# Kernel tuning notes

Measured on AMD Instinct MI355X. Metric: run time of the kernel, lower is better.

Reference implementation:

```python
import jax, jax.numpy as jnp
import numpy as np

B, N, E, H = 8, 2000, 20, 128


def setup_inputs() -> dict:
    key = jax.random.key(0)
    ks = jax.random.split(key, 9)
    s = 1.0 / np.sqrt(H)
    return {
        "x": jax.random.normal(ks[0], (B, N, H), dtype=jnp.float32),
        "e": jax.random.normal(ks[1], (B, N * E, H), dtype=jnp.float32),
        "Wu": jax.random.uniform(ks[2], (H, H), jnp.float32, -s, s),
        "bu": jax.random.uniform(ks[3], (H,), jnp.float32, -s, s),
        "Wv": jax.random.uniform(ks[4], (H, H), jnp.float32, -s, s),
        "bv": jax.random.uniform(ks[5], (H,), jnp.float32, -s, s),
        "We": jax.random.uniform(ks[6], (H, H), jnp.float32, -s, s),
        "be": jax.random.uniform(ks[7], (H,), jnp.float32, -s, s),
        "edge_index": jax.random.randint(ks[8], (B, N * E), 0, N, dtype=jnp.int32),
        "n_edges": E,
    }


def reference(x, e, Wu, bu, Wv, bv, We, be, edge_index, n_edges):
    b, n, h = x.shape
    Ux = x @ Wu + bu                      # [B, N, H] node self-embedding
    Vx = x @ Wv + bv                      # [B, N, H] neighbor embedding
    Ve = e @ We + be                      # [B, N*E, H] edge embedding
    # softmax over the n_edges axis per (node, channel)
    Ve = jax.nn.softmax(Ve.reshape(b, n, n_edges, h), axis=2)
    # gather neighbor features along node axis via edge_index
    Vx_g = jnp.take_along_axis(Vx, edge_index[..., None], axis=1)  # [B, N*E, H]
    to = (Ve * Vx_g.reshape(b, n, n_edges, h)).sum(axis=2)          # [B, N, H]
    return Ux + to
```

## Files before the change

kernel.cpp:

```cpp
#include <hip/hip_runtime.h>

#define B_   8
#define NN   2000
#define EE   20
#define HH   128
#define BN   (B_*NN)
#define NE   (NN*EE)

typedef unsigned short ushort_t;
typedef __bf16 bf16x8 __attribute__((ext_vector_type(8)));
typedef float  f32x4  __attribute__((ext_vector_type(4)));
typedef float  f4     __attribute__((ext_vector_type(4)));
typedef unsigned short us8 __attribute__((ext_vector_type(8)));
typedef unsigned short us4 __attribute__((ext_vector_type(4)));

union FragU { us8 u; bf16x8 b; };

__device__ __forceinline__ float b2f(ushort_t v) {
    union { unsigned int i; float f; } c; c.i = ((unsigned int)v) << 16; return c.f;
}
__device__ __forceinline__ ushort_t f2b(float f) {
    union { float f; unsigned int i; } c; c.f = f;
    unsigned int r = (c.i + 0x7FFFu + ((c.i >> 16) & 1u)) >> 16;
    return (ushort_t)r;
}

__global__ __launch_bounds__(256) void k0_prep(
    const float* __restrict__ x,
    const float* __restrict__ Wu, const float* __restrict__ Wv,
    const float* __restrict__ We,
    ushort_t* __restrict__ xb,
    ushort_t* __restrict__ WuT, ushort_t* __restrict__ WvT,
    ushort_t* __restrict__ WeT)
{
    const int bid = blockIdx.x;
    if (bid < 125) {
        const size_t base = (size_t)bid * 128 * HH;
#pragma unroll
        for (int it = 0; it < 16; ++it) {
            int c = it * 256 + threadIdx.x;
            size_t off = base + (size_t)c * 4;
            f4 v = *(const f4*)(x + off);
            us4 pk;
#pragma unroll
            for (int r = 0; r < 4; ++r) pk[r] = f2b(v[r]);
            *(us4*)(xb + off) = pk;
        }
    } else {
        const float* W = (bid == 125) ? Wu : (bid == 126) ? Wv : We;
        ushort_t*   WT = (bid == 125) ? WuT : (bid == 126) ? WvT : WeT;
#pragma unroll
        for (int it = 0; it < 64; ++it) {
            int c = it * 256 + threadIdx.x;
            int k = c >> 7, n = c & 127;
            WT[n * HH + k] = f2b(W[c]);
        }
    }
}

__global__ __launch_bounds__(256, 4) void k1_embed(
    const ushort_t* __restrict__ xb,
    const ushort_t* __restrict__ WuT, const float* __restrict__ bu,
    const ushort_t* __restrict__ WvT, const float* __restrict__ bv,
    ushort_t* __restrict__ Uxb, ushort_t* __restrict__ Vxb)
{
    const int tid  = threadIdx.x;
    const int lane = tid & 63;
    const int wave = tid >> 6;
    const int wm = wave >> 1, wn = wave & 1;
    const int q  = lane >> 4, ln = lane & 15;
    const int m0 = blockIdx.x * 64;
    const int sel = blockIdx.y;
    const ushort_t* WT   = sel ? WvT : WuT;
    const float*    bias = sel ? bv : bu;
    ushort_t* dst = sel ? Vxb : Uxb;

    f32x4 acc[2][4];
#pragma unroll
    for (int tm = 0; tm < 2; ++tm)
#pragma unroll
        for (int tn = 0; tn < 4; ++tn) acc[tm][tn] = (f32x4){0.f, 0.f, 0.f, 0.f};

#pragma unroll
    for (int ki = 0; ki < 4; ++ki) {
        FragU af[2], bf[4];
#pragma unroll
        for (int tm = 0; tm < 2; ++tm)
            af[tm].u = *(const us8*)(xb + (size_t)(m0 + wm * 32 + tm * 16 + ln) * HH + ki * 32 + q * 8);
#pragma unroll
        for (int tn = 0; tn < 4; ++tn)
            bf[tn].u = *(const us8*)(WT + (size_t)(wn * 64 + tn * 16 + ln) * HH + ki * 32 + q * 8);
#pragma unroll
        for (int tm = 0; tm < 2; ++tm)
#pragma unroll
            for (int tn = 0; tn < 4; ++tn)
                acc[tm][tn] = __builtin_amdgcn_mfma_f32_16x16x32_bf16(
                    af[tm].b, bf[tn].b, acc[tm][tn], 0, 0, 0);
    }

#pragma unroll
    for (int tn = 0; tn < 4; ++tn) {
        int col = wn * 64 + tn * 16 + ln;
        float bb = bias[col];
#pragma unroll
        for (int tm = 0; tm < 2; ++tm) {
            int rowb = m0 + wm * 32 + tm * 16 + q * 4;
#pragma unroll
            for (int r = 0; r < 4; ++r)
                dst[(size_t)(rowb + r) * HH + col] = f2b(acc[tm][tn][r] + bb);
        }
    }
}

#define ASTR 136
#define CSTR 84

__global__ __launch_bounds__(256, 4) void k2_fused(
    const float* __restrict__ e, const ushort_t* __restrict__ WeT,
    const int* __restrict__ eidx,
    const ushort_t* __restrict__ Uxb, const ushort_t* __restrict__ Vxb,
    float* __restrict__ out)
{
    __shared__ __align__(16) ushort_t smem[11008];
    __shared__ int sidx[80];

    const int tid  = threadIdx.x;
    const int lane = tid & 63;
    const int wave = tid >> 6;
    const int q  = lane >> 4, ln = lane & 15;

    const int b   = blockIdx.y;
    const int nl0 = blockIdx.x * 4;
    const size_t erow0 = (size_t)b * NE + (size_t)nl0 * EE;

#pragma unroll
    for (int it = 0; it < 10; ++it) {
        int c = it * 256 + tid;
        int row = c >> 5, col = (c & 31) * 4;
        f4 v = *(const f4*)(e + (erow0 + row) * HH + col);
        us4 pk;
#pragma unroll
        for (int r = 0; r < 4; ++r) pk[r] = f2b(v[r]);
        *(us4*)(&smem[row * ASTR + col]) = pk;
    }
    if (tid < 80) sidx[tid] = eidx[erow0 + tid];

    FragU bf[4][2];
#pragma unroll
    for (int ki = 0; ki < 4; ++ki)
#pragma unroll
        for (int tn = 0; tn < 2; ++tn)
            bf[ki][tn].u = *(const us8*)(WeT + (size_t)(wave * 32 + tn * 16 + ln) * HH + ki * 32 + q * 8);

    f32x4 acc[5][2];
#pragma unroll
    for (int tm = 0; tm < 5; ++tm)
#pragma unroll
        for (int tn = 0; tn < 2; ++tn) acc[tm][tn] = (f32x4){0.f, 0.f, 0.f, 0.f};

    __syncthreads();

#pragma unroll
    for (int ki = 0; ki < 4; ++ki) {
        FragU af[5];
#pragma unroll
        for (int tm = 0; tm < 5; ++tm)
            af[tm].u = *(const us8*)(&smem[(tm * 16 + ln) * ASTR + ki * 32 + q * 8]);
#pragma unroll
        for (int tm = 0; tm < 5; ++tm)
#pragma unroll
            for (int tn = 0; tn < 2; ++tn)
                acc[tm][tn] = __builtin_amdgcn_mfma_f32_16x16x32_bf16(
                    af[tm].b, bf[ki][tn].b, acc[tm][tn], 0, 0, 0);
    }

    __syncthreads();

#pragma unroll
    for (int tm = 0; tm < 5; ++tm)
#pragma unroll
        for (int tn = 0; tn < 2; ++tn) {
            int col  = wave * 32 + tn * 16 + ln;
            int rowb = tm * 16 + q * 4;
            us4 pk;
#pragma unroll
            for (int r = 0; r < 4; ++r) pk[r] = f2b(acc[tm][tn][r]);
            *(us4*)(&smem[col * CSTR + rowb]) = pk;
        }


    const int hh = lane & 31;
    const int gh = lane >> 5;
    const int h  = wave * 32 + hh;
    const ushort_t* vbase = Vxb + (size_t)b * NN * HH + h;
#pragma unroll
    for (int j = 0; j < 2; ++j) {
        int g = gh + 2 * j;
        const ushort_t* ctp = &smem[h * CSTR + g * 20];
        float lv[20];
#pragma unroll
        for (int i = 0; i < 5; ++i) {
            us4 v = *(const us4*)(ctp + i * 4);
#pragma unroll
            for (int r = 0; r < 4; ++r) lv[i * 4 + r] = b2f(v[r]);
        }
        float mx = lv[0];
#pragma unroll
        for (int k = 1; k < EE; ++k) mx = fmaxf(mx, lv[k]);

        ushort_t gv[20];
        const int ib = g * 20;
#pragma unroll
        for (int k = 0; k < EE; ++k)
            gv[k] = vbase[(size_t)sidx[ib + k] * HH];

        float s = 0.f, a = 0.f;
#pragma unroll
        for (int k = 0; k < EE; ++k) {
            float p = __expf(lv[k] - mx);
            s += p;
            a = fmaf(p, b2f(gv[k]), a);
        }
        size_t orow = (size_t)(b * NN + nl0 + g) * HH + h;
        out[orow] = b2f(Uxb[orow]) + a / s;
    }
}

extern "C" void kernel_launch(void* const* d_in, const int* in_sizes, int n_in,
                              void* d_out, int out_size, void* d_ws, size_t ws_size,
                              hipStream_t stream) {
    const float* x  = (const float*)d_in[0];
    const float* e  = (const float*)d_in[1];
    const float* Wu = (const float*)d_in[2];
    const float* bu = (const float*)d_in[3];
    const float* Wv = (const float*)d_in[4];
    const float* bv = (const float*)d_in[5];
    const float* We = (const float*)d_in[6];
    const int*   eidx = (const int*)d_in[8];

    const size_t SZ = (size_t)BN * HH * 2;
    ushort_t* Uxb = (ushort_t*)d_ws;
    ushort_t* Vxb = (ushort_t*)((char*)d_ws + SZ);
    ushort_t* xb  = (ushort_t*)((char*)d_ws + 2 * SZ);
    ushort_t* WuT = (ushort_t*)((char*)d_ws + 3 * SZ);
    ushort_t* WvT = WuT + HH * HH;
    ushort_t* WeT = WvT + HH * HH;
    float*    o   = (float*)d_out;

    k0_prep<<<dim3(128), 256, 0, stream>>>(x, Wu, Wv, We, xb, WuT, WvT, WeT);
    k1_embed<<<dim3(250, 2), 256, 0, stream>>>(xb, WuT, bu, WvT, bv, Uxb, Vxb);
    k2_fused<<<dim3(500, 8), 256, 0, stream>>>(e, WeT, eidx, Uxb, Vxb, o);
}
```

Before: 283.2 us.

## Load fp32 activations directly into MFMA fragments, drop x conversion and LDS staging

```diff
diff --git a/kernel.cpp b/kernel.cpp
--- a/kernel.cpp
+++ b/kernel.cpp
@@ -26,40 +26,30 @@
 }
 
 __global__ __launch_bounds__(256) void k0_prep(
-    const float* __restrict__ x,
     const float* __restrict__ Wu, const float* __restrict__ Wv,
     const float* __restrict__ We,
-    ushort_t* __restrict__ xb,
     ushort_t* __restrict__ WuT, ushort_t* __restrict__ WvT,
     ushort_t* __restrict__ WeT)
 {
+    __shared__ ushort_t lds[128 * 130];
     const int bid = blockIdx.x;
-    if (bid < 125) {
-        const size_t base = (size_t)bid * 128 * HH;
-#pragma unroll
-        for (int it = 0; it < 16; ++it) {
-            int c = it * 256 + threadIdx.x;
-            size_t off = base + (size_t)c * 4;
-            f4 v = *(const f4*)(x + off);
-            us4 pk;
-#pragma unroll
-            for (int r = 0; r < 4; ++r) pk[r] = f2b(v[r]);
-            *(us4*)(xb + off) = pk;
-        }
-    } else {
-        const float* W = (bid == 125) ? Wu : (bid == 126) ? Wv : We;
-        ushort_t*   WT = (bid == 125) ? WuT : (bid == 126) ? WvT : WeT;
-#pragma unroll
-        for (int it = 0; it < 64; ++it) {
-            int c = it * 256 + threadIdx.x;
-            int k = c >> 7, n = c & 127;
-            WT[n * HH + k] = f2b(W[c]);
-        }
+    const float* W = (bid == 0) ? Wu : (bid == 1) ? Wv : We;
+    ushort_t*   WT = (bid == 0) ? WuT : (bid == 1) ? WvT : WeT;
+#pragma unroll
+    for (int it = 0; it < 64; ++it) {
+        int c = it * 256 + threadIdx.x;
+        lds[(c >> 7) * 130 + (c & 127)] = f2b(W[c]);
+    }
+    __syncthreads();
+#pragma unroll
+    for (int it = 0; it < 64; ++it) {
+        int o = it * 256 + threadIdx.x;
+        WT[o] = lds[(o & 127) * 130 + (o >> 7)];
     }
 }
 
 __global__ __launch_bounds__(256, 4) void k1_embed(
-    const ushort_t* __restrict__ xb,
+    const float* __restrict__ x,
     const ushort_t* __restrict__ WuT, const float* __restrict__ bu,
     const ushort_t* __restrict__ WvT, const float* __restrict__ bv,
     ushort_t* __restrict__ Uxb, ushort_t* __restrict__ Vxb)
@@ -75,6 +65,13 @@
     const float*    bias = sel ? bv : bu;
     ushort_t* dst = sel ? Vxb : Uxb;
 
+    FragU bf[4][4];
+#pragma unroll
+    for (int ki = 0; ki < 4; ++ki)
+#pragma unroll
+        for (int tn = 0; tn < 4; ++tn)
+            bf[ki][tn].u = *(const us8*)(WT + (size_t)(wn * 64 + tn * 16 + ln) * HH + ki * 32 + q * 8);
+
     f32x4 acc[2][4];
 #pragma unroll
     for (int tm = 0; tm < 2; ++tm)
@@ -83,19 +80,23 @@
 
 #pragma unroll
     for (int ki = 0; ki < 4; ++ki) {
-        FragU af[2], bf[4];
-#pragma unroll
-        for (int tm = 0; tm < 2; ++tm)
-            af[tm].u = *(const us8*)(xb + (size_t)(m0 + wm * 32 + tm * 16 + ln) * HH + ki * 32 + q * 8);
-#pragma unroll
-        for (int tn = 0; tn < 4; ++tn)
-            bf[tn].u = *(const us8*)(WT + (size_t)(wn * 64 + tn * 16 + ln) * HH + ki * 32 + q * 8);
+        FragU af[2];
+#pragma unroll
+        for (int tm = 0; tm < 2; ++tm) {
+            const float* p = x + (size_t)(m0 + wm * 32 + tm * 16 + ln) * HH + ki * 32 + q * 8;
+            f4 lo = *(const f4*)(p);
+            f4 hi = *(const f4*)(p + 4);
+            us8 t;
+#pragma unroll
+            for (int r = 0; r < 4; ++r) { t[r] = f2b(lo[r]); t[r + 4] = f2b(hi[r]); }
+            af[tm].u = t;
+        }
 #pragma unroll
         for (int tm = 0; tm < 2; ++tm)
 #pragma unroll
             for (int tn = 0; tn < 4; ++tn)
                 acc[tm][tn] = __builtin_amdgcn_mfma_f32_16x16x32_bf16(
-                    af[tm].b, bf[tn].b, acc[tm][tn], 0, 0, 0);
+                    af[tm].b, bf[ki][tn].b, acc[tm][tn], 0, 0, 0);
     }
 
 #pragma unroll
@@ -112,7 +113,6 @@
     }
 }
 
-#define ASTR 136
 #define CSTR 84
 
 __global__ __launch_bounds__(256, 4) void k2_fused(
@@ -121,8 +121,7 @@
     const ushort_t* __restrict__ Uxb, const ushort_t* __restrict__ Vxb,
     float* __restrict__ out)
 {
-    __shared__ __align__(16) ushort_t smem[11008];
-    __shared__ int sidx[80];
+    __shared__ __align__(16) ushort_t ct[128 * CSTR];
 
     const int tid  = threadIdx.x;
     const int lane = tid & 63;
@@ -132,18 +131,7 @@
     const int b   = blockIdx.y;
     const int nl0 = blockIdx.x * 4;
     const size_t erow0 = (size_t)b * NE + (size_t)nl0 * EE;
-
-#pragma unroll
-    for (int it = 0; it < 10; ++it) {
-        int c = it * 256 + tid;
-        int row = c >> 5, col = (c & 31) * 4;
-        f4 v = *(const f4*)(e + (erow0 + row) * HH + col);
-        us4 pk;
-#pragma unroll
-        for (int r = 0; r < 4; ++r) pk[r] = f2b(v[r]);
-        *(us4*)(&smem[row * ASTR + col]) = pk;
-    }
-    if (tid < 80) sidx[tid] = eidx[erow0 + tid];
+    const float* ebase = e + erow0 * HH;
 
     FragU bf[4][2];
 #pragma unroll
@@ -158,14 +146,19 @@
 #pragma unroll
         for (int tn = 0; tn < 2; ++tn) acc[tm][tn] = (f32x4){0.f, 0.f, 0.f, 0.f};
 
-    __syncthreads();
-
 #pragma unroll
     for (int ki = 0; ki < 4; ++ki) {
         FragU af[5];
 #pragma unroll
-        for (int tm = 0; tm < 5; ++tm)
-            af[tm].u = *(const us8*)(&smem[(tm * 16 + ln) * ASTR + ki * 32 + q * 8]);
+        for (int tm = 0; tm < 5; ++tm) {
+            const float* p = ebase + (size_t)(tm * 16 + ln) * HH + ki * 32 + q * 8;
+            f4 lo = *(const f4*)(p);
+            f4 hi = *(const f4*)(p + 4);
+            us8 t;
+#pragma unroll
+            for (int r = 0; r < 4; ++r) { t[r] = f2b(lo[r]); t[r + 4] = f2b(hi[r]); }
+            af[tm].u = t;
+        }
 #pragma unroll
         for (int tm = 0; tm < 5; ++tm)
 #pragma unroll
@@ -173,8 +166,6 @@
                 acc[tm][tn] = __builtin_amdgcn_mfma_f32_16x16x32_bf16(
                     af[tm].b, bf[ki][tn].b, acc[tm][tn], 0, 0, 0);
     }
-
-    __syncthreads();
 
 #pragma unroll
     for (int tm = 0; tm < 5; ++tm)
@@ -185,18 +176,18 @@
             us4 pk;
 #pragma unroll
             for (int r = 0; r < 4; ++r) pk[r] = f2b(acc[tm][tn][r]);
-            *(us4*)(&smem[col * CSTR + rowb]) = pk;
-        }
-
+            *(us4*)(&ct[col * CSTR + rowb]) = pk;
+        }
 
     const int hh = lane & 31;
     const int gh = lane >> 5;
     const int h  = wave * 32 + hh;
     const ushort_t* vbase = Vxb + (size_t)b * NN * HH + h;
+    const int* ebidx = eidx + erow0;
 #pragma unroll
     for (int j = 0; j < 2; ++j) {
         int g = gh + 2 * j;
-        const ushort_t* ctp = &smem[h * CSTR + g * 20];
+        const ushort_t* ctp = &ct[h * CSTR + g * 20];
         float lv[20];
 #pragma unroll
         for (int i = 0; i < 5; ++i) {
@@ -208,11 +199,12 @@
 #pragma unroll
         for (int k = 1; k < EE; ++k) mx = fmaxf(mx, lv[k]);
 
+        int idx[20];
+#pragma unroll
+        for (int k = 0; k < EE; ++k) idx[k] = ebidx[g * 20 + k];
         ushort_t gv[20];
-        const int ib = g * 20;
-#pragma unroll
-        for (int k = 0; k < EE; ++k)
-            gv[k] = vbase[(size_t)sidx[ib + k] * HH];
+#pragma unroll
+        for (int k = 0; k < EE; ++k) gv[k] = vbase[(size_t)idx[k] * HH];
 
         float s = 0.f, a = 0.f;
 #pragma unroll
@@ -241,13 +233,12 @@
     const size_t SZ = (size_t)BN * HH * 2;
     ushort_t* Uxb = (ushort_t*)d_ws;
     ushort_t* Vxb = (ushort_t*)((char*)d_ws + SZ);
-    ushort_t* xb  = (ushort_t*)((char*)d_ws + 2 * SZ);
-    ushort_t* WuT = (ushort_t*)((char*)d_ws + 3 * SZ);
+    ushort_t* WuT = (ushort_t*)((char*)d_ws + 2 * SZ);
     ushort_t* WvT = WuT + HH * HH;
     ushort_t* WeT = WvT + HH * HH;
     float*    o   = (float*)d_out;
 
-    k0_prep<<<dim3(128), 256, 0, stream>>>(x, Wu, Wv, We, xb, WuT, WvT, WeT);
-    k1_embed<<<dim3(250, 2), 256, 0, stream>>>(xb, WuT, bu, WvT, bv, Uxb, Vxb);
+    k0_prep<<<dim3(3), 256, 0, stream>>>(Wu, Wv, We, WuT, WvT, WeT);
+    k1_embed<<<dim3(250, 2), 256, 0, stream>>>(x, WuT, bu, WvT, bv, Uxb, Vxb);
     k2_fused<<<dim3(500, 8), 256, 0, stream>>>(e, WeT, eidx, Uxb, Vxb, o);
 }
```

New measurement: 308.9 us. 1.09x slower.
